# Optimization experiments

Measured on AMD Instinct MI355X. Metric: run time of the kernel, lower is better.

The kernel has to match this reference:

```python
import jax, jax.numpy as jnp
import numpy as np

B, T, C, V = 4, 2048, 512, 32000


def setup_inputs() -> dict:
    key = jax.random.key(0)
    ks = jax.random.split(key, 8)
    return {
        "idx": jax.random.randint(ks[0], (B, T), 0, V, dtype=jnp.int64 if jax.config.jax_enable_x64 else jnp.int32),
        "targets": jax.random.randint(ks[1], (B, T), 0, V, dtype=jnp.int64 if jax.config.jax_enable_x64 else jnp.int32),
        "token_emb": jax.random.normal(ks[2], (V, C), jnp.float32) * 0.02,
        "pos_emb": jax.random.normal(ks[3], (T, C), jnp.float32) * 0.02,
        "Wk": jax.random.normal(ks[4], (C, C), jnp.float32) / np.sqrt(C),
        "Wq": jax.random.normal(ks[5], (C, C), jnp.float32) / np.sqrt(C),
        "Wv": jax.random.normal(ks[6], (C, C), jnp.float32) / np.sqrt(C),
        "Wo": jax.random.normal(ks[7], (C, V), jnp.float32) / np.sqrt(C),
        "bo": jnp.zeros((V,), jnp.float32),
    }


def reference(idx, targets, token_emb, pos_emb, Wk, Wq, Wv, Wo, bo):
    # embeddings: token lookup + positional add  -> [B, T, C]
    x = token_emb[idx] + pos_emb[None, :idx.shape[1]]
    # single self-attention head (scale uses input dim C, per source)
    q = x @ Wq  # [B, T, C]
    k = x @ Wk
    v = x @ Wv
    wei = jnp.einsum("btc,bsc->bts", q, k) * (C ** -0.5)  # [B, T, T]
    mask = jnp.tril(jnp.ones((idx.shape[1], idx.shape[1]), bool))
    wei = jnp.where(mask[None], wei, -jnp.inf)
    wei = jax.nn.softmax(wei, axis=-1)
    attn = jnp.einsum("bts,bsc->btc", wei, v)  # [B, T, C]
    logits = attn @ Wo + bo  # [B, T, V]
    # cross-entropy (mean over B*T), matching F.cross_entropy
    logp = jax.nn.log_softmax(logits, axis=-1)
    nll = -jnp.take_along_axis(logp, targets[..., None], axis=-1)[..., 0]
    loss = nll.mean()
    return logits, loss
```

## Files before the change

kernel.cpp:

```cpp
#include <hip/hip_runtime.h>
#include <cstdint>

typedef unsigned short u16;
typedef __attribute__((ext_vector_type(8))) short short8;
typedef __attribute__((ext_vector_type(4))) float f32x4;

constexpr int kB = 4, kT = 2048, kC = 512, kV = 32000;
constexpr int kBT = kB * kT;
constexpr float kScale = 0.044194173824159216f;

__device__ __forceinline__ u16 f2b(float f) {
  union { float f; unsigned u; } v; v.f = f;
  unsigned r = v.u + 0x7fffu + ((v.u >> 16) & 1u);
  return (u16)(r >> 16);
}

__device__ __forceinline__ void g2lds16(const u16* g, u16* l) {
  __builtin_amdgcn_global_load_lds(
      (const __attribute__((address_space(1))) void*)g,
      (__attribute__((address_space(3))) void*)l, 16, 0, 0);
}

__global__ __launch_bounds__(256) void transpose_cast(const float* __restrict__ in,
                                                      u16* __restrict__ out,
                                                      int R, int Ncol) {
  __shared__ u16 tile[32][33];
  int c0 = blockIdx.x * 32, r0 = blockIdx.y * 32;
  int tx = threadIdx.x, ty = threadIdx.y;
#pragma unroll
  for (int j = 0; j < 32; j += 8)
    tile[ty + j][tx] = f2b(in[(long)(r0 + ty + j) * Ncol + (c0 + tx)]);
  __syncthreads();
#pragma unroll
  for (int j = 0; j < 32; j += 8)
    out[(long)(c0 + ty + j) * R + (r0 + tx)] = tile[tx][ty + j];
}

__global__ __launch_bounds__(128) void embed_kernel(const int* __restrict__ idx,
                                                    const float* __restrict__ te,
                                                    const float* __restrict__ pe,
                                                    u16* __restrict__ xb) {
  int row = blockIdx.x;
  int t = row & (kT - 1);
  int tok = idx[row];
  int c = threadIdx.x * 4;
  float4 a = *(const float4*)(te + (long)tok * kC + c);
  float4 p = *(const float4*)(pe + (long)t * kC + c);
  ushort4 o;
  o.x = f2b(a.x + p.x); o.y = f2b(a.y + p.y);
  o.z = f2b(a.z + p.z); o.w = f2b(a.w + p.w);
  *(ushort4*)(xb + (long)row * kC + c) = o;
}

template <int OUT_MODE, bool CAUSAL, bool KCAP>
__global__ __launch_bounds__(256) void gemm_bt(
    const u16* __restrict__ A, const u16* __restrict__ Bt, void* __restrict__ OutP,
    const float* __restrict__ bias,
    int M, int N, int K, int lda, int ldb, int ldo,
    long batchA, long batchB, long batchO, float alpha) {
  int bz = blockIdx.z;
  A += bz * batchA;
  Bt += bz * batchB;
  int m0 = blockIdx.y * 128, n0 = blockIdx.x * 128;
  if (CAUSAL && n0 > m0 + 127) return;

  __shared__ u16 As[2][128 * 32];
  __shared__ u16 Bs[2][128 * 32];
  int tid = threadIdx.x;
  int lane = tid & 63, w = tid >> 6;
  int wr = w >> 1, wc = w & 1;
  int lm = lane & 15, lk = lane >> 4;

  f32x4 acc[4][4] = {};

  const u16* aptr = A + (long)(m0 + (w << 4) + (lane >> 2)) * lda + ((lane & 3) << 3);
  const u16* bptr = Bt + (long)(n0 + (w << 4) + (lane >> 2)) * ldb + ((lane & 3) << 3);

#define STAGE(buf)                                                   \
  {                                                                  \
    g2lds16(aptr,                  &As[buf][(w << 4) * 32]);         \
    g2lds16(aptr + (long)64 * lda, &As[buf][(64 + (w << 4)) * 32]);  \
    g2lds16(bptr,                  &Bs[buf][(w << 4) * 32]);         \
    g2lds16(bptr + (long)64 * ldb, &Bs[buf][(64 + (w << 4)) * 32]);  \
  }

  int nk = K >> 5;
  if (KCAP) { int cap = (m0 >> 5) + 4; nk = (cap < nk) ? cap : nk; }
  STAGE(0);
  __syncthreads();

  for (int kt = 0; kt < nk; ++kt) {
    int cur = kt & 1;
    aptr += 32; bptr += 32;
    if (kt + 1 < nk) STAGE(cur ^ 1);
    short8 af[4], bf[4];
#pragma unroll
    for (int i = 0; i < 4; ++i) {
      af[i] = *(const short8*)&As[cur][(wr * 64 + i * 16 + lm) * 32 + lk * 8];
      bf[i] = *(const short8*)&Bs[cur][(wc * 64 + i * 16 + lm) * 32 + lk * 8];
    }
#pragma unroll
    for (int mi = 0; mi < 4; ++mi)
#pragma unroll
      for (int ni = 0; ni < 4; ++ni)
        acc[mi][ni] = __builtin_amdgcn_mfma_f32_16x16x32_bf16(af[mi], bf[ni], acc[mi][ni], 0, 0, 0);
    __syncthreads();
  }
#undef STAGE

#pragma unroll
  for (int mi = 0; mi < 4; ++mi) {
#pragma unroll
    for (int ni = 0; ni < 4; ++ni) {
      int row = m0 + wr * 64 + mi * 16 + lk * 4;
      int col = n0 + wc * 64 + ni * 16 + lm;
      if (OUT_MODE == 0) {
        float* Out = (float*)OutP + bz * batchO;
        float bv = bias ? bias[col] : 0.0f;
#pragma unroll
        for (int r = 0; r < 4; ++r)
          Out[(long)(row + r) * ldo + col] = acc[mi][ni][r] * alpha + bv;
      } else if (OUT_MODE == 1) {
        u16* Out = (u16*)OutP + bz * batchO;
#pragma unroll
        for (int r = 0; r < 4; ++r)
          Out[(long)(row + r) * ldo + col] = f2b(acc[mi][ni][r] * alpha);
      } else {
        u16* Out = (u16*)OutP + bz * batchO;
        ushort4 pk;
        pk.x = f2b(acc[mi][ni][0] * alpha);
        pk.y = f2b(acc[mi][ni][1] * alpha);
        pk.z = f2b(acc[mi][ni][2] * alpha);
        pk.w = f2b(acc[mi][ni][3] * alpha);
        *(ushort4*)&Out[(long)col * ldo + row] = pk;
      }
    }
  }
}

__global__ __launch_bounds__(512, 2) void gemm256_logits_ce(
    const u16* __restrict__ A, const u16* __restrict__ Bt,
    float* __restrict__ Out, const float* __restrict__ bias,
    float2* __restrict__ cepart) {
  constexpr int lda = kC, ldb = kC, ldo = kV;
  constexpr int nk = kC / 64;
  constexpr int NB = kV / 256;

  __shared__ u16 lds[65536];

  int wg = blockIdx.x;
  int xcd = wg & 7;
  int i = wg >> 3;
  int g = i >> 5, r = i & 31;
  int bx = (g < 15) ? (g * 8 + (r >> 2)) : (120 + (r >> 2));
  int by = xcd * 4 + (r & 3);
  int m0 = by * 256, n0 = bx * 256;

  int tid = threadIdx.x;
  int lane = tid & 63, w = tid >> 6;
  int wm = w >> 2, wn = w & 3;
  int lm = lane & 15, lk = lane >> 4;
  int lk16 = lk * 16, sw = (lm & 7) << 4;
  int brow0 = (wn & 1) * 64;

  int srow = tid >> 3;
  int scol = ((tid & 7) ^ ((tid >> 3) & 7)) * 8;
  const u16* Arow = A + (long)(m0 + srow) * lda + scol;
  const u16* Brow = Bt + (long)(n0 + srow) * ldb + scol;

  f32x4 acc[8][4] = {};
  short8 aF[4][2], bF[4][2];

  auto stage = [&](int s) {
    if (s >= 4 * nk) return;
    int tile = s >> 2, hf = s & 3, buf = tile & 1;
    int kofs = tile * 64;
    if (hf >= 2) {
      u16* base = &lds[(buf * 2 + (hf - 2)) * 8192 + w * 512];
      const u16* gp = Arow + (long)((hf - 2) * 128) * lda + kofs;
      g2lds16(gp, base);
      g2lds16(gp + (long)64 * lda, base + 4096);
    } else {
      u16* base = &lds[32768 + (buf * 2 + hf) * 8192 + w * 512];
      const u16* gp = Brow + (long)(hf * 128) * ldb + kofs;
      g2lds16(gp, base);
      g2lds16(gp + (long)64 * ldb, base + 4096);
    }
  };

#pragma unroll
  for (int s = 0; s < 6; ++s) stage(s);
  asm volatile("s_waitcnt vmcnt(4)" ::: "memory");
  __builtin_amdgcn_sched_barrier(0);
  __builtin_amdgcn_s_barrier();

#pragma unroll 2
  for (int t = 0; t < nk; ++t) {
    int cur = t & 1;
    const char* Ab = (const char*)&lds[(cur * 2 + wm) * 8192];
    const char* Bb = (const char*)&lds[32768 + (cur * 2 + (wn >> 1)) * 8192];

#define RDA(i, ks) (*(const short8*)(Ab + (((qr)*4 + (i)) * 16 + lm) * 128 + (((ks)*64 + lk16) ^ sw)))
#define RDB(j, ks) (*(const short8*)(Bb + (brow0 + ((qc)*2 + (j)) * 16 + lm) * 128 + (((ks)*64 + lk16) ^ sw)))
#define MFMA_QUAD                                                              \
  _Pragma("unroll") for (int i = 0; i < 4; ++i)                                \
  _Pragma("unroll") for (int j = 0; j < 2; ++j)                                \
  _Pragma("unroll") for (int ks = 0; ks < 2; ++ks)                             \
      acc[qr * 4 + i][qc * 2 + j] = __builtin_amdgcn_mfma_f32_16x16x32_bf16(   \
          aF[i][ks], bF[qc * 2 + j][ks], acc[qr * 4 + i][qc * 2 + j], 0, 0, 0);

    {
      constexpr int qr = 0, qc = 0;
#pragma unroll
      for (int i = 0; i < 4; ++i) { aF[i][0] = RDA(i, 0); aF[i][1] = RDA(i, 1); }
#pragma unroll
      for (int j = 0; j < 2; ++j) { bF[j][0] = RDB(j, 0); bF[j][1] = RDB(j, 1); }
      stage(4 * (t + 1) + 2);
      stage(4 * (t + 1) + 3);
      __builtin_amdgcn_s_barrier();
      asm volatile("s_waitcnt lgkmcnt(0)" ::: "memory");
      __builtin_amdgcn_s_setprio(1);
      MFMA_QUAD
      __builtin_amdgcn_s_setprio(0);
      __builtin_amdgcn_s_barrier();
    }
    {
      constexpr int qr = 0, qc = 1;
#pragma unroll
      for (int j = 0; j < 2; ++j) { bF[2 + j][0] = RDB(j, 0); bF[2 + j][1] = RDB(j, 1); }
      __builtin_amdgcn_s_barrier();
      asm volatile("s_waitcnt lgkmcnt(0)" ::: "memory");
      __builtin_amdgcn_s_setprio(1);
      MFMA_QUAD
      __builtin_amdgcn_s_setprio(0);
      __builtin_amdgcn_s_barrier();
    }
    {
      constexpr int qr = 1, qc = 0;
#pragma unroll
      for (int i = 0; i < 4; ++i) { aF[i][0] = RDA(i, 0); aF[i][1] = RDA(i, 1); }
      __builtin_amdgcn_s_barrier();
      asm volatile("s_waitcnt lgkmcnt(0)" ::: "memory");
      __builtin_amdgcn_s_setprio(1);
      MFMA_QUAD
      __builtin_amdgcn_s_setprio(0);
      __builtin_amdgcn_s_barrier();
    }
    {
      constexpr int qr = 1, qc = 1;
      stage(4 * (t + 2) + 0);
      stage(4 * (t + 2) + 1);
      __builtin_amdgcn_s_barrier();
      asm volatile("s_waitcnt lgkmcnt(0)" ::: "memory");
      __builtin_amdgcn_s_setprio(1);
      MFMA_QUAD
      __builtin_amdgcn_s_setprio(0);
      if (t < nk - 2) {
        asm volatile("s_waitcnt vmcnt(4)" ::: "memory");
        __builtin_amdgcn_sched_barrier(0);
      } else if (t == nk - 2) {
        asm volatile("s_waitcnt vmcnt(0)" ::: "memory");
        __builtin_amdgcn_sched_barrier(0);
      }
      __builtin_amdgcn_s_barrier();
    }
#undef RDA
#undef RDB
#undef MFMA_QUAD
  }

  float2* lds_ce = (float2*)lds;
#pragma unroll
  for (int rf = 0; rf < 8; ++rf) {
    int grow = m0 + wm * 128 + rf * 16 + lk * 4;
    float rm[4], rs[4];
#pragma unroll
    for (int r = 0; r < 4; ++r) { rm[r] = -1e30f; rs[r] = 0.0f; }
#pragma unroll
    for (int cf = 0; cf < 4; ++cf) {
      int col = n0 + wn * 64 + cf * 16 + lm;
      float bv = bias[col];
#pragma unroll
      for (int r = 0; r < 4; ++r) {
        float v = acc[rf][cf][r] + bv;
        __builtin_nontemporal_store(v, &Out[(long)(grow + r) * ldo + col]);
        float M = fmaxf(rm[r], v);
        rs[r] = rs[r] * __expf(rm[r] - M) + __expf(v - M);
        rm[r] = M;
      }
    }
#pragma unroll
    for (int off = 1; off < 16; off <<= 1) {
#pragma unroll
      for (int r = 0; r < 4; ++r) {
        float om = __shfl_xor(rm[r], off, 64);
        float os = __shfl_xor(rs[r], off, 64);
        float M = fmaxf(rm[r], om);
        rs[r] = rs[r] * __expf(rm[r] - M) + os * __expf(om - M);
        rm[r] = M;
      }
    }
    if (lm == 0) {
#pragma unroll
      for (int r = 0; r < 4; ++r)
        lds_ce[w * 128 + rf * 16 + lk * 4 + r] = make_float2(rm[r], rs[r]);
    }
  }
  __syncthreads();
  if (tid < 256) {
    int row = tid, wmg = row >> 7, r128 = row & 127;
    float m = -1e30f, s = 0.0f;
#pragma unroll
    for (int j = 0; j < 4; ++j) {
      float2 v = lds_ce[(wmg * 4 + j) * 128 + r128];
      float M = fmaxf(m, v.x);
      s = s * __expf(m - M) + v.y * __expf(v.x - M);
      m = M;
    }
    cepart[(long)(m0 + row) * NB + bx] = make_float2(m, s);
  }
}

__global__ __launch_bounds__(256) void softmax_causal(const float* __restrict__ S,
                                                      u16* __restrict__ P) {
  int row = blockIdx.x;
  int t = row & (kT - 1);
  int lim = ((t >> 7) + 1) << 7;
  const float* srow = S + (long)row * kT;
  u16* prow = P + (long)row * kT;
  __shared__ float buf[kT];
  __shared__ float red[256];
  int tid = threadIdx.x;
  float mx = -1e30f;
  for (int s = tid; s < lim; s += 256) {
    float v = (s <= t) ? srow[s] : -1e30f;
    buf[s] = v;
    mx = fmaxf(mx, v);
  }
  red[tid] = mx; __syncthreads();
  for (int o = 128; o > 0; o >>= 1) {
    if (tid < o) red[tid] = fmaxf(red[tid], red[tid + o]);
    __syncthreads();
  }
  mx = red[0]; __syncthreads();
  float sm = 0.0f;
  for (int s = tid; s < lim; s += 256) {
    float e = (s <= t) ? __expf(buf[s] - mx) : 0.0f;
    buf[s] = e;
    sm += e;
  }
  red[tid] = sm; __syncthreads();
  for (int o = 128; o > 0; o >>= 1) {
    if (tid < o) red[tid] += red[tid + o];
    __syncthreads();
  }
  float inv = 1.0f / red[0];
  for (int s = tid; s < lim; s += 256) prow[s] = f2b(buf[s] * inv);
}

__global__ __launch_bounds__(256) void ce_reduce(const float* __restrict__ logits,
                                                 const float2* __restrict__ part,
                                                 const int* __restrict__ targets,
                                                 float* __restrict__ nll, int P) {
  int row = blockIdx.x * 4 + (threadIdx.x >> 6);
  int lane = threadIdx.x & 63;
  const float2* pr = part + (long)row * P;
  float m = -1e30f, s = 0.0f;
  for (int p = lane; p < P; p += 64) {
    float2 v = pr[p];
    float M = fmaxf(m, v.x);
    s = s * __expf(m - M) + v.y * __expf(v.x - M);
    m = M;
  }
#pragma unroll
  for (int off = 1; off < 64; off <<= 1) {
    float om = __shfl_xor(m, off, 64), os = __shfl_xor(s, off, 64);
    float M = fmaxf(m, om);
    s = s * __expf(m - M) + os * __expf(om - M);
    m = M;
  }
  if (lane == 0) {
    float lse = m + __logf(s);
    nll[row] = lse - logits[(long)row * kV + targets[row]];
  }
}

__global__ __launch_bounds__(256) void loss_reduce(const float* __restrict__ nll,
                                                   float* __restrict__ out) {
  __shared__ float red[256];
  int tid = threadIdx.x;
  float s = 0.0f;
  for (int i = tid; i < kBT; i += 256) s += nll[i];
  red[tid] = s; __syncthreads();
  for (int o = 128; o > 0; o >>= 1) {
    if (tid < o) red[tid] += red[tid + o];
    __syncthreads();
  }
  if (tid == 0) out[0] = red[0] / (float)kBT;
}

extern "C" void kernel_launch(void* const* d_in, const int* in_sizes, int n_in,
                              void* d_out, int out_size, void* d_ws, size_t ws_size,
                              hipStream_t stream) {
  const int* idx       = (const int*)d_in[0];
  const int* targets   = (const int*)d_in[1];
  const float* token_e = (const float*)d_in[2];
  const float* pos_e   = (const float*)d_in[3];
  const float* Wk      = (const float*)d_in[4];
  const float* Wq      = (const float*)d_in[5];
  const float* Wv      = (const float*)d_in[6];
  const float* Wo      = (const float*)d_in[7];
  const float* bo      = (const float*)d_in[8];
  float* out = (float*)d_out;

  char* ws = (char*)d_ws;
  size_t need = 0;
  auto alloc = [&](size_t bytes) { char* p = ws + need; need += (bytes + 255) & ~(size_t)255; return p; };
  u16* xb   = (u16*)alloc((size_t)kBT * kC * 2);
  u16* wqt  = (u16*)alloc((size_t)kC * kC * 2);
  u16* wkt  = (u16*)alloc((size_t)kC * kC * 2);
  u16* wvt  = (u16*)alloc((size_t)kC * kC * 2);
  u16* wot  = (u16*)alloc((size_t)kV * kC * 2);
  u16* qb   = (u16*)alloc((size_t)kBT * kC * 2);
  u16* kb   = (u16*)alloc((size_t)kBT * kC * 2);
  u16* vt   = (u16*)alloc((size_t)kC * kBT * 2);
  u16* attn = (u16*)alloc((size_t)kBT * kC * 2);
  float* nll = (float*)alloc((size_t)kBT * 4);
  if (ws_size < need) return;

  float2* cepart = (float2*)qb;

  float* Sbuf = out;
  u16* Pbuf   = (u16*)((char*)d_out + (100ull << 20));

  dim3 tb(32, 8);
  transpose_cast<<<dim3(kC / 32, kC / 32), tb, 0, stream>>>(Wq, wqt, kC, kC);
  transpose_cast<<<dim3(kC / 32, kC / 32), tb, 0, stream>>>(Wk, wkt, kC, kC);
  transpose_cast<<<dim3(kC / 32, kC / 32), tb, 0, stream>>>(Wv, wvt, kC, kC);
  transpose_cast<<<dim3(kV / 32, kC / 32), tb, 0, stream>>>(Wo, wot, kC, kV);

  embed_kernel<<<kBT, 128, 0, stream>>>(idx, token_e, pos_e, xb);

  gemm_bt<1, false, false><<<dim3(4, 64, 2), 256, 0, stream>>>(xb, wqt, qb, nullptr,
      kBT, kC, kC, kC, kC, kC, 0, (long)kC * kC, (long)kBT * kC, 1.0f);
  gemm_bt<2, false, false><<<dim3(4, 64, 1), 256, 0, stream>>>(xb, wvt, vt, nullptr,
      kBT, kC, kC, kC, kC, kBT, 0, 0, 0, 1.0f);

  gemm_bt<0, true, false><<<dim3(16, 16, 4), 256, 0, stream>>>(qb, kb, Sbuf, nullptr,
      kT, kT, kC, kC, kC, kT, (long)kT * kC, (long)kT * kC, (long)kT * kT, kScale);

  softmax_causal<<<kBT, 256, 0, stream>>>(Sbuf, Pbuf);

  gemm_bt<1, false, true><<<dim3(4, 16, 4), 256, 0, stream>>>(Pbuf, vt, attn, nullptr,
      kT, kC, kT, kT, kBT, kC, (long)kT * kT, (long)kT, (long)kT * kC, 1.0f);

  gemm256_logits_ce<<<dim3((kV / 256) * (kBT / 256)), 512, 0, stream>>>(
      attn, wot, out, bo, cepart);

  ce_reduce<<<kBT / 4, 256, 0, stream>>>(out, cepart, targets, nll, kV / 256);
  loss_reduce<<<1, 256, 0, stream>>>(nll, out + (long)kBT * kV);
}
```

Baseline: 611.6 us.

## Retile logits+CE GEMM to 256x128 tiles with K=32 steps and higher occupancy

Replaces the 256x256, K=64 logits GEMM with a 256x128 tile and a 32-wide K step. LDS shrinks to 48KB and launch bounds ask for 4 blocks per CU, aiming to raise occupancy and hide latency. The price is lower data reuse per tile, twice as many K iterations and barriers, and no LDS swizzle, so bank conflicts are possible. CE partials per row double to 250, so more work lands in ce_reduce, and a tighter register cap could cause spills.

```diff
diff --git a/kernel.cpp b/kernel.cpp
--- a/kernel.cpp
+++ b/kernel.cpp
@@ -138,125 +138,92 @@
   }
 }
 
-__global__ __launch_bounds__(512, 2) void gemm256_logits_ce(
+__global__ __launch_bounds__(512, 4) void gemm_logits_ce(
     const u16* __restrict__ A, const u16* __restrict__ Bt,
     float* __restrict__ Out, const float* __restrict__ bias,
     float2* __restrict__ cepart) {
   constexpr int lda = kC, ldb = kC, ldo = kV;
-  constexpr int nk = kC / 64;
-  constexpr int NB = kV / 256;
-
-  __shared__ u16 lds[65536];
+  constexpr int nk = kC / 32;
+  constexpr int NBce = kV / 128;
+
+  __shared__ u16 lds[24576];
 
   int wg = blockIdx.x;
   int xcd = wg & 7;
   int i = wg >> 3;
-  int g = i >> 5, r = i & 31;
-  int bx = (g < 15) ? (g * 8 + (r >> 2)) : (120 + (r >> 2));
-  int by = xcd * 4 + (r & 3);
-  int m0 = by * 256, n0 = bx * 256;
+  int by = xcd * 4 + (i & 3);
+  int bx = i >> 2;
+  int m0 = by * 256, n0 = bx * 128;
 
   int tid = threadIdx.x;
   int lane = tid & 63, w = tid >> 6;
   int wm = w >> 2, wn = w & 3;
   int lm = lane & 15, lk = lane >> 4;
-  int lk16 = lk * 16, sw = (lm & 7) << 4;
-  int brow0 = (wn & 1) * 64;
-
-  int srow = tid >> 3;
-  int scol = ((tid & 7) ^ ((tid >> 3) & 7)) * 8;
-  const u16* Arow = A + (long)(m0 + srow) * lda + scol;
-  const u16* Brow = Bt + (long)(n0 + srow) * ldb + scol;
-
-  f32x4 acc[8][4] = {};
-  short8 aF[4][2], bF[4][2];
-
-  auto stage = [&](int s) {
-    if (s >= 4 * nk) return;
-    int tile = s >> 2, hf = s & 3, buf = tile & 1;
-    int kofs = tile * 64;
-    if (hf >= 2) {
-      u16* base = &lds[(buf * 2 + (hf - 2)) * 8192 + w * 512];
-      const u16* gp = Arow + (long)((hf - 2) * 128) * lda + kofs;
-      g2lds16(gp, base);
-      g2lds16(gp + (long)64 * lda, base + 4096);
-    } else {
-      u16* base = &lds[32768 + (buf * 2 + hf) * 8192 + w * 512];
-      const u16* gp = Brow + (long)(hf * 128) * ldb + kofs;
-      g2lds16(gp, base);
-      g2lds16(gp + (long)64 * ldb, base + 4096);
-    }
+
+  int srow = tid >> 2;
+  int schunk = (tid & 3) * 8;
+  const u16* Arow = A + (long)(m0 + srow) * lda + schunk;
+  const u16* Brow = Bt + (long)(n0 + srow) * ldb + schunk;
+
+  f32x4 acc[8][2] = {};
+  short8 aF[4], bF[2];
+
+  auto stageA = [&](int tile, int half) {
+    if (tile >= nk) return;
+    u16* base = &lds[(tile & 1) * 8192 + half * 4096 + w * 512];
+    g2lds16(Arow + (long)half * 128 * lda + tile * 32, base);
   };
-
-#pragma unroll
-  for (int s = 0; s < 6; ++s) stage(s);
-  asm volatile("s_waitcnt vmcnt(4)" ::: "memory");
+  auto stageB = [&](int tile) {
+    if (tile >= nk) return;
+    u16* base = &lds[16384 + (tile & 1) * 4096 + w * 512];
+    g2lds16(Brow + tile * 32, base);
+  };
+
+  stageA(0, 0); stageA(0, 1); stageB(0); stageB(1);
+  asm volatile("s_waitcnt vmcnt(1)" ::: "memory");
   __builtin_amdgcn_sched_barrier(0);
   __builtin_amdgcn_s_barrier();
 
 #pragma unroll 2
   for (int t = 0; t < nk; ++t) {
     int cur = t & 1;
-    const char* Ab = (const char*)&lds[(cur * 2 + wm) * 8192];
-    const char* Bb = (const char*)&lds[32768 + (cur * 2 + (wn >> 1)) * 8192];
-
-#define RDA(i, ks) (*(const short8*)(Ab + (((qr)*4 + (i)) * 16 + lm) * 128 + (((ks)*64 + lk16) ^ sw)))
-#define RDB(j, ks) (*(const short8*)(Bb + (brow0 + ((qc)*2 + (j)) * 16 + lm) * 128 + (((ks)*64 + lk16) ^ sw)))
-#define MFMA_QUAD                                                              \
-  _Pragma("unroll") for (int i = 0; i < 4; ++i)                                \
-  _Pragma("unroll") for (int j = 0; j < 2; ++j)                                \
-  _Pragma("unroll") for (int ks = 0; ks < 2; ++ks)                             \
-      acc[qr * 4 + i][qc * 2 + j] = __builtin_amdgcn_mfma_f32_16x16x32_bf16(   \
-          aF[i][ks], bF[qc * 2 + j][ks], acc[qr * 4 + i][qc * 2 + j], 0, 0, 0);
+    const char* Ab = (const char*)lds + cur * 16384 + wm * 8192;
+    const char* Bb = (const char*)lds + 32768 + cur * 8192;
+
+#define RDA(rf) (*(const short8*)(Ab + (((rf)*16 + lm) * 64) + lk * 16))
+#define RDB(cf) (*(const short8*)(Bb + ((wn * 32 + (cf)*16 + lm) * 64) + lk * 16))
 
     {
-      constexpr int qr = 0, qc = 0;
-#pragma unroll
-      for (int i = 0; i < 4; ++i) { aF[i][0] = RDA(i, 0); aF[i][1] = RDA(i, 1); }
-#pragma unroll
-      for (int j = 0; j < 2; ++j) { bF[j][0] = RDB(j, 0); bF[j][1] = RDB(j, 1); }
-      stage(4 * (t + 1) + 2);
-      stage(4 * (t + 1) + 3);
+#pragma unroll
+      for (int rf = 0; rf < 4; ++rf) aF[rf] = RDA(rf);
+      bF[0] = RDB(0); bF[1] = RDB(1);
+      stageA(t + 1, 0); stageA(t + 1, 1);
       __builtin_amdgcn_s_barrier();
       asm volatile("s_waitcnt lgkmcnt(0)" ::: "memory");
       __builtin_amdgcn_s_setprio(1);
-      MFMA_QUAD
+#pragma unroll
+      for (int rf = 0; rf < 4; ++rf)
+#pragma unroll
+        for (int cf = 0; cf < 2; ++cf)
+          acc[rf][cf] = __builtin_amdgcn_mfma_f32_16x16x32_bf16(aF[rf], bF[cf], acc[rf][cf], 0, 0, 0);
       __builtin_amdgcn_s_setprio(0);
       __builtin_amdgcn_s_barrier();
     }
     {
-      constexpr int qr = 0, qc = 1;
-#pragma unroll
-      for (int j = 0; j < 2; ++j) { bF[2 + j][0] = RDB(j, 0); bF[2 + j][1] = RDB(j, 1); }
+#pragma unroll
+      for (int rf = 0; rf < 4; ++rf) aF[rf] = RDA(rf + 4);
+      stageB(t + 2);
       __builtin_amdgcn_s_barrier();
       asm volatile("s_waitcnt lgkmcnt(0)" ::: "memory");
       __builtin_amdgcn_s_setprio(1);
-      MFMA_QUAD
-      __builtin_amdgcn_s_setprio(0);
-      __builtin_amdgcn_s_barrier();
-    }
-    {
-      constexpr int qr = 1, qc = 0;
-#pragma unroll
-      for (int i = 0; i < 4; ++i) { aF[i][0] = RDA(i, 0); aF[i][1] = RDA(i, 1); }
-      __builtin_amdgcn_s_barrier();
-      asm volatile("s_waitcnt lgkmcnt(0)" ::: "memory");
-      __builtin_amdgcn_s_setprio(1);
-      MFMA_QUAD
-      __builtin_amdgcn_s_setprio(0);
-      __builtin_amdgcn_s_barrier();
-    }
-    {
-      constexpr int qr = 1, qc = 1;
-      stage(4 * (t + 2) + 0);
-      stage(4 * (t + 2) + 1);
-      __builtin_amdgcn_s_barrier();
-      asm volatile("s_waitcnt lgkmcnt(0)" ::: "memory");
-      __builtin_amdgcn_s_setprio(1);
-      MFMA_QUAD
+#pragma unroll
+      for (int rf = 0; rf < 4; ++rf)
+#pragma unroll
+        for (int cf = 0; cf < 2; ++cf)
+          acc[rf + 4][cf] = __builtin_amdgcn_mfma_f32_16x16x32_bf16(aF[rf], bF[cf], acc[rf + 4][cf], 0, 0, 0);
       __builtin_amdgcn_s_setprio(0);
       if (t < nk - 2) {
-        asm volatile("s_waitcnt vmcnt(4)" ::: "memory");
+        asm volatile("s_waitcnt vmcnt(1)" ::: "memory");
         __builtin_amdgcn_sched_barrier(0);
       } else if (t == nk - 2) {
         asm volatile("s_waitcnt vmcnt(0)" ::: "memory");
@@ -266,7 +233,6 @@
     }
 #undef RDA
 #undef RDB
-#undef MFMA_QUAD
   }
 
   float2* lds_ce = (float2*)lds;
@@ -277,8 +243,8 @@
 #pragma unroll
     for (int r = 0; r < 4; ++r) { rm[r] = -1e30f; rs[r] = 0.0f; }
 #pragma unroll
-    for (int cf = 0; cf < 4; ++cf) {
-      int col = n0 + wn * 64 + cf * 16 + lm;
+    for (int cf = 0; cf < 2; ++cf) {
+      int col = n0 + wn * 32 + cf * 16 + lm;
       float bv = bias[col];
 #pragma unroll
       for (int r = 0; r < 4; ++r) {
@@ -303,12 +269,12 @@
     if (lm == 0) {
 #pragma unroll
       for (int r = 0; r < 4; ++r)
-        lds_ce[w * 128 + rf * 16 + lk * 4 + r] = make_float2(rm[r], rs[r]);
+        lds_ce[(wm * 4 + wn) * 128 + rf * 16 + lk * 4 + r] = make_float2(rm[r], rs[r]);
     }
   }
   __syncthreads();
   if (tid < 256) {
-    int row = tid, wmg = row >> 7, r128 = row & 127;
+    int wmg = tid >> 7, r128 = tid & 127;
     float m = -1e30f, s = 0.0f;
 #pragma unroll
     for (int j = 0; j < 4; ++j) {
@@ -317,7 +283,7 @@
       s = s * __expf(m - M) + v.y * __expf(v.x - M);
       m = M;
     }
-    cepart[(long)(m0 + row) * NB + bx] = make_float2(m, s);
+    cepart[(long)(m0 + tid) * NBce + bx] = make_float2(m, s);
   }
 }
 
@@ -454,9 +420,9 @@
   gemm_bt<1, false, true><<<dim3(4, 16, 4), 256, 0, stream>>>(Pbuf, vt, attn, nullptr,
       kT, kC, kT, kT, kBT, kC, (long)kT * kT, (long)kT, (long)kT * kC, 1.0f);
 
-  gemm256_logits_ce<<<dim3((kV / 256) * (kBT / 256)), 512, 0, stream>>>(
+  gemm_logits_ce<<<dim3((kBT / 256) * (kV / 128)), 512, 0, stream>>>(
       attn, wot, out, bo, cepart);
 
-  ce_reduce<<<kBT / 4, 256, 0, stream>>>(out, cepart, targets, nll, kV / 256);
+  ce_reduce<<<kBT / 4, 256, 0, stream>>>(out, cepart, targets, nll, kV / 128);
   loss_reduce<<<1, 256, 0, stream>>>(nll, out + (long)kBT * kV);
 }
```

New measurement: 655.9 us. +7.2%, slower.
